# Kernel tuning notes

Measured on AMD Instinct MI355X. Metric: run time of the kernel, lower is better.

Reference implementation:

```python
import jax, jax.numpy as jnp
import numpy as np

INPUT_SIZE = 1024
HIDDEN_SIZE = 1024
BATCH = 8192


def setup_inputs() -> dict:
    key = jax.random.key(0)
    ks = jax.random.split(key, 14)
    stdv = 1.0 / HIDDEN_SIZE ** 0.5
    u = lambda k, shape: jax.random.uniform(k, shape, jnp.float32, -stdv, stdv)
    H, I = HIDDEN_SIZE, INPUT_SIZE
    return {
        "x": jax.random.normal(ks[0], (BATCH, I), jnp.float32),
        "hidden": jax.random.normal(ks[1], (BATCH, H), jnp.float32),
        "weight_xr": u(ks[2], (H, I)),
        "weight_hr": u(ks[3], (H, H)),
        "bias_r": u(ks[4], (H,)),
        "weight_xz": u(ks[5], (H, I)),
        "weight_hz": u(ks[6], (H, H)),
        "bias_z": u(ks[7], (H,)),
        "weight_xh": u(ks[8], (H, I)),
        "weight_hh": u(ks[9], (H, H)),
        "bias_h": u(ks[10], (H,)),
        "weight_c": u(ks[11], (H, I + H)),
        "bias_c": u(ks[12], (H,)),
        "weight_hat_h": u(ks[13], (H, I + H)),
        "bias_hat_h": u(jax.random.fold_in(key, 99), (H,)),
    }


def reference(x, hidden, weight_xr, weight_hr, bias_r, weight_xz, weight_hz, bias_z,
              weight_xh, weight_hh, bias_h, weight_c, bias_c, weight_hat_h, bias_hat_h):
    # combined: [B, I+H]
    combined = jnp.concatenate([x, hidden], axis=1)
    c_t = combined @ weight_c.T + bias_c                      # [B, H]
    a_t = jax.nn.softmax(c_t, axis=1)
    hat_h_t = a_t * jax.nn.relu(combined @ weight_hat_h.T + bias_hat_h)
    r_t = jax.nn.sigmoid(x @ weight_xr.T + bias_r + hidden @ weight_hr.T)
    z_t = jax.nn.sigmoid(x @ weight_xz.T + bias_z + hidden @ weight_hz.T)
    h_tilde = jnp.tanh(x @ weight_xh.T + bias_h + (r_t * hidden) @ weight_hh.T)
    h_t = (1.0 - z_t) * h_tilde + z_t * hidden + hat_h_t
    return h_t
```

## Files before the change

kernel.cpp:

```cpp
#include <hip/hip_runtime.h>

typedef unsigned short ushort_t;
typedef __attribute__((ext_vector_type(8))) short short8;
typedef __attribute__((ext_vector_type(4))) float float4v;
typedef __attribute__((ext_vector_type(4))) ushort_t ushort4v;

#define B_ROWS 8192
#define HDIM   1024
#define GLD    5120

__device__ __forceinline__ float bf2f(ushort_t u) {
    return __uint_as_float(((unsigned)u) << 16);
}
__device__ __forceinline__ ushort_t f2bf(float f) {
    unsigned u = __float_as_uint(f);
    u += 0x7FFFu + ((u >> 16) & 1u);
    return (ushort_t)(u >> 16);
}

__global__ __launch_bounds__(256) void pack_all(
    const float* __restrict__ x, const float* __restrict__ h,
    const float* __restrict__ wc, const float* __restrict__ what,
    const float* __restrict__ wxr, const float* __restrict__ whr,
    const float* __restrict__ wxz, const float* __restrict__ whz,
    const float* __restrict__ wxh, const float* __restrict__ whh,
    ushort_t* __restrict__ A, ushort_t* __restrict__ W,
    ushort_t* __restrict__ Whh)
{
    const int bid = blockIdx.x;
    float4v v;
    ushort_t* dst;
    size_t i4;
    if (bid < 16384) {
        i4 = ((size_t)bid * 256 + threadIdx.x) * 4;
        int c = (int)(i4 & 2047);
        size_t b = i4 >> 11;
        const float* src = (c < 1024) ? (x + b * 1024 + c)
                                      : (h + b * 1024 + (c - 1024));
        v = *(const float4v*)src;
        dst = A + i4;
    } else if (bid < 26624) {
        i4 = ((size_t)(bid - 16384) * 256 + threadIdx.x) * 4;
        int j = (int)(i4 >> 11);
        int k = (int)(i4 & 2047);
        int r = j >> 10, jr = j & 1023;
        if (r == 0) {
            v = *(const float4v*)(wc + (size_t)j * 2048 + k);
        } else if (r == 1) {
            v = *(const float4v*)(what + (size_t)jr * 2048 + k);
        } else if (r == 4) {
            v = (k < 1024) ? *(const float4v*)(wxh + (size_t)jr * 1024 + k)
                           : (float4v){0.f, 0.f, 0.f, 0.f};
        } else {
            const float* p0 = (r == 2) ? wxr : wxz;
            const float* p1 = (r == 2) ? whr : whz;
            const float* p = (k < 1024) ? (p0 + (size_t)jr * 1024 + k)
                                        : (p1 + (size_t)jr * 1024 + (k - 1024));
            v = *(const float4v*)p;
        }
        dst = W + i4;
    } else {
        i4 = ((size_t)(bid - 26624) * 256 + threadIdx.x) * 4;
        v = *(const float4v*)(whh + i4);
        dst = Whh + i4;
    }
    ushort4v o;
#pragma unroll
    for (int t = 0; t < 4; ++t) o[t] = f2bf(v[t]);
    *(ushort4v*)dst = o;
}

__global__ __launch_bounds__(256, 2) void gemm1(
    const ushort_t* __restrict__ A, const ushort_t* __restrict__ B,
    ushort_t* __restrict__ C)
{
    const int bn0 = blockIdx.x * 128;
    const int bm0 = blockIdx.y * 256;
    const int K = (bn0 >= 4096) ? 1024 : 2048;

    __shared__ ushort_t As[256 * 64];
    __shared__ ushort_t Bs[128 * 64];

    const int t = threadIdx.x;
    const int wave = t >> 6, lane = t & 63;
    const int q = lane >> 4, r16 = lane & 15;
    const int lrow8 = lane >> 3;
    const int kswz = ((lane & 7) ^ lrow8) * 8;
    const int xm = (r16 & 7);

    float4v acc[4][8];
#pragma unroll
    for (int i = 0; i < 4; ++i)
#pragma unroll
        for (int j = 0; j < 8; ++j)
            acc[i][j] = {0.f, 0.f, 0.f, 0.f};

    for (int k0 = 0; k0 < K; k0 += 64) {
#pragma unroll
        for (int j = 0; j < 8; ++j) {
            int l = wave * 8 + j;
            const ushort_t* gp = A + (size_t)(bm0 + l * 8 + lrow8) * 2048 + k0 + kswz;
            __builtin_amdgcn_global_load_lds(
                (const __attribute__((address_space(1))) void*)gp,
                (__attribute__((address_space(3))) void*)(As + l * 512),
                16, 0, 0);
        }
#pragma unroll
        for (int j = 0; j < 4; ++j) {
            int l = wave * 4 + j;
            const ushort_t* gp = B + (size_t)(bn0 + l * 8 + lrow8) * 2048 + k0 + kswz;
            __builtin_amdgcn_global_load_lds(
                (const __attribute__((address_space(1))) void*)gp,
                (__attribute__((address_space(3))) void*)(Bs + l * 512),
                16, 0, 0);
        }
        __syncthreads();

#pragma unroll
        for (int kh = 0; kh < 2; ++kh) {
            short8 af[4];
#pragma unroll
            for (int mi = 0; mi < 4; ++mi)
                af[mi] = *(const short8*)
                    &As[(wave * 64 + mi * 16 + r16) * 64 + (((kh * 4 + q) ^ xm) * 8)];
#pragma unroll
            for (int ni = 0; ni < 8; ++ni) {
                short8 bf = *(const short8*)
                    &Bs[(ni * 16 + r16) * 64 + (((kh * 4 + q) ^ xm) * 8)];
#pragma unroll
                for (int mi = 0; mi < 4; ++mi)
                    acc[mi][ni] = __builtin_amdgcn_mfma_f32_16x16x32_bf16(
                        af[mi], bf, acc[mi][ni], 0, 0, 0);
            }
        }
        __syncthreads();
    }

#pragma unroll
    for (int mi = 0; mi < 4; ++mi)
#pragma unroll
        for (int ni = 0; ni < 8; ++ni)
#pragma unroll
            for (int reg = 0; reg < 4; ++reg) {
                int row = bm0 + wave * 64 + mi * 16 + q * 4 + reg;
                int col = bn0 + ni * 16 + r16;
                C[(size_t)row * GLD + col] = f2bf(acc[mi][ni][reg]);
            }
}

__global__ __launch_bounds__(256) void row_pass(
    ushort_t* __restrict__ G, const float* __restrict__ bias_c,
    const float* __restrict__ bias_hat, const float* __restrict__ bias_r,
    const float* __restrict__ hidden, ushort_t* __restrict__ rh)
{
    const int wave = threadIdx.x >> 6, lane = threadIdx.x & 63;
    const size_t row = (size_t)blockIdx.x * 4 + wave;
    ushort_t* g = G + row * GLD;
    const int c0 = lane * 16;

    float cv[16];
    {
        short8 a = *(const short8*)(g + c0);
        short8 b = *(const short8*)(g + c0 + 8);
#pragma unroll
        for (int i = 0; i < 8; ++i) {
            cv[i]     = bf2f((ushort_t)a[i]) + bias_c[c0 + i];
            cv[8 + i] = bf2f((ushort_t)b[i]) + bias_c[c0 + 8 + i];
        }
    }
    float mx = cv[0];
#pragma unroll
    for (int i = 1; i < 16; ++i) mx = fmaxf(mx, cv[i]);
#pragma unroll
    for (int m = 1; m < 64; m <<= 1) mx = fmaxf(mx, __shfl_xor(mx, m));
    float sum = 0.f;
#pragma unroll
    for (int i = 0; i < 16; ++i) { cv[i] = __expf(cv[i] - mx); sum += cv[i]; }
#pragma unroll
    for (int m = 1; m < 64; m <<= 1) sum += __shfl_xor(sum, m);
    const float inv = 1.0f / sum;

    {
        short8 a = *(const short8*)(g + 1024 + c0);
        short8 b = *(const short8*)(g + 1024 + c0 + 8);
        short8 oa, ob;
#pragma unroll
        for (int i = 0; i < 8; ++i) {
            float ha = bf2f((ushort_t)a[i]) + bias_hat[c0 + i];
            float hb = bf2f((ushort_t)b[i]) + bias_hat[c0 + 8 + i];
            oa[i] = (short)f2bf(cv[i] * inv * fmaxf(ha, 0.f));
            ob[i] = (short)f2bf(cv[8 + i] * inv * fmaxf(hb, 0.f));
        }
        *(short8*)(g + c0) = oa;
        *(short8*)(g + c0 + 8) = ob;
    }

    {
        short8 a = *(const short8*)(g + 2048 + c0);
        short8 b = *(const short8*)(g + 2048 + c0 + 8);
        const float* hp = hidden + row * 1024 + c0;
        short8 oa, ob;
#pragma unroll
        for (int i = 0; i < 8; ++i) {
            float ra = 1.0f / (1.0f + __expf(-(bf2f((ushort_t)a[i]) + bias_r[c0 + i])));
            float rb = 1.0f / (1.0f + __expf(-(bf2f((ushort_t)b[i]) + bias_r[c0 + 8 + i])));
            oa[i] = (short)f2bf(ra * hp[i]);
            ob[i] = (short)f2bf(rb * hp[8 + i]);
        }
        ushort_t* rp = rh + row * 1024 + c0;
        *(short8*)rp = oa;
        *(short8*)(rp + 8) = ob;
    }
}

#define CSTRIDE 132
__global__ __launch_bounds__(256) void gemm2_final(
    const ushort_t* __restrict__ A, const ushort_t* __restrict__ B,
    const ushort_t* __restrict__ G, const float* __restrict__ bias_z,
    const float* __restrict__ bias_h, const float* __restrict__ hidden,
    float* __restrict__ out)
{
    const int bn0 = blockIdx.x * 128;
    const int bm0 = blockIdx.y * 64;

    __shared__ ushort_t smem[64 * CSTRIDE];
    ushort_t* As = smem;
    ushort_t* Bs = smem + 2048;

    const int t = threadIdx.x;
    const int wave = t >> 6, lane = t & 63;
    const int wr = wave >> 1, wcq = wave & 1;
    const int q = lane >> 4, r16 = lane & 15;
    const int lrow = lane >> 2;
    const int lcol = (lane & 3) * 8;

    float4v acc[2][4];
#pragma unroll
    for (int i = 0; i < 2; ++i)
#pragma unroll
        for (int j = 0; j < 4; ++j)
            acc[i][j] = {0.f, 0.f, 0.f, 0.f};

    for (int k0 = 0; k0 < 1024; k0 += 32) {
#pragma unroll
        for (int j = 0; j < 3; ++j) {
            int l = wave * 3 + j;
            if (l < 4) {
                const ushort_t* gp = A + (size_t)(bm0 + l * 16 + lrow) * 1024 + k0 + lcol;
                __builtin_amdgcn_global_load_lds(
                    (const __attribute__((address_space(1))) void*)gp,
                    (__attribute__((address_space(3))) void*)(As + l * 512),
                    16, 0, 0);
            } else {
                const ushort_t* gp = B + (size_t)(bn0 + (l - 4) * 16 + lrow) * 1024 + k0 + lcol;
                __builtin_amdgcn_global_load_lds(
                    (const __attribute__((address_space(1))) void*)gp,
                    (__attribute__((address_space(3))) void*)(Bs + (l - 4) * 512),
                    16, 0, 0);
            }
        }
        __syncthreads();

        short8 af[2], bf[4];
#pragma unroll
        for (int mi = 0; mi < 2; ++mi)
            af[mi] = *(const short8*)&As[(wr * 32 + mi * 16 + r16) * 32 + q * 8];
#pragma unroll
        for (int ni = 0; ni < 4; ++ni)
            bf[ni] = *(const short8*)&Bs[(wcq * 64 + ni * 16 + r16) * 32 + q * 8];
#pragma unroll
        for (int mi = 0; mi < 2; ++mi)
#pragma unroll
            for (int ni = 0; ni < 4; ++ni)
                acc[mi][ni] = __builtin_amdgcn_mfma_f32_16x16x32_bf16(
                    af[mi], bf[ni], acc[mi][ni], 0, 0, 0);
        __syncthreads();
    }

#pragma unroll
    for (int mi = 0; mi < 2; ++mi)
#pragma unroll
        for (int ni = 0; ni < 4; ++ni)
#pragma unroll
            for (int reg = 0; reg < 4; ++reg) {
                int rl = wr * 32 + mi * 16 + q * 4 + reg;
                int cl = wcq * 64 + ni * 16 + r16;
                smem[rl * CSTRIDE + cl] = f2bf(acc[mi][ni][reg]);
            }
    __syncthreads();

    const int colL = t & 127;
    const int gc = bn0 + colL;
    const float bz = bias_z[gc];
    const float bh = bias_h[gc];
    const int rbase = t >> 7;
#pragma unroll 4
    for (int pass = 0; pass < 32; ++pass) {
        const int rowL = pass * 2 + rbase;
        const size_t gr = (size_t)(bm0 + rowL);
        const ushort_t* grow = G + gr * GLD;
        float z = 1.0f / (1.0f + __expf(-(bf2f(grow[3072 + gc]) + bz)));
        float targ = bf2f(grow[4096 + gc]) + bh + bf2f(smem[rowL * CSTRIDE + colL]);
        float th = 1.0f - 2.0f / (__expf(2.0f * targ) + 1.0f);
        out[gr * 1024 + gc] =
            (1.0f - z) * th + z * hidden[gr * 1024 + gc] + bf2f(grow[gc]);
    }
}


extern "C" void kernel_launch(void* const* d_in, const int* in_sizes, int n_in,
                              void* d_out, int out_size, void* d_ws, size_t ws_size,
                              hipStream_t stream)
{
    const float* x        = (const float*)d_in[0];
    const float* hidden   = (const float*)d_in[1];
    const float* wxr      = (const float*)d_in[2];
    const float* whr      = (const float*)d_in[3];
    const float* bias_r   = (const float*)d_in[4];
    const float* wxz      = (const float*)d_in[5];
    const float* whz      = (const float*)d_in[6];
    const float* bias_z   = (const float*)d_in[7];
    const float* wxh      = (const float*)d_in[8];
    const float* whh      = (const float*)d_in[9];
    const float* bias_h   = (const float*)d_in[10];
    const float* wc       = (const float*)d_in[11];
    const float* bias_c   = (const float*)d_in[12];
    const float* what     = (const float*)d_in[13];
    const float* bias_hat = (const float*)d_in[14];
    float* out = (float*)d_out;

    char* ws = (char*)d_ws;
    ushort_t* G     = (ushort_t*)(ws);
    ushort_t* Abf   = (ushort_t*)(ws + 83886080);
    ushort_t* Wbf   = (ushort_t*)(ws + 117440512);
    ushort_t* Whhbf = (ushort_t*)(ws + 138412032);
    ushort_t* rhbf  = (ushort_t*)(ws + 140509184);

    pack_all<<<27648, 256, 0, stream>>>(x, hidden, wc, what, wxr, whr, wxz, whz,
                                        wxh, whh, Abf, Wbf, Whhbf);

    gemm1<<<dim3(40, 32), 256, 0, stream>>>(Abf, Wbf, G);

    row_pass<<<B_ROWS / 4, 256, 0, stream>>>(G, bias_c, bias_hat, bias_r, hidden, rhbf);

    gemm2_final<<<dim3(8, 128), 256, 0, stream>>>(rhbf, Whhbf, G, bias_z, bias_h,
                                                  hidden, out);
}
```

Measured before the change: 376.3 us.

## Fuse r-gate epilogue into gemm1, stage stores via LDS, enlarge gemm2 tiles

gemm1 now stages its accumulator tile through shared memory so each thread writes 128-byte contiguous rows instead of scattered 2-byte stores. For the r-gate column block it computes sigmoid(r)*hidden directly and writes rh, so it no longer stores that slice of G and row_pass no longer reads it back. gemm2_final moves to 128x128 tiles with K-step 64 and XOR-swizzled LDS loads, which raises reuse per block but halves the grid and adds register pressure.

```diff
diff --git a/kernel.cpp b/kernel.cpp
--- a/kernel.cpp
+++ b/kernel.cpp
@@ -70,16 +70,19 @@
     *(ushort4v*)dst = o;
 }
 
+#define CS1 136
 __global__ __launch_bounds__(256, 2) void gemm1(
     const ushort_t* __restrict__ A, const ushort_t* __restrict__ B,
-    ushort_t* __restrict__ C)
+    ushort_t* __restrict__ C, const float* __restrict__ hidden,
+    const float* __restrict__ bias_r, ushort_t* __restrict__ rh)
 {
     const int bn0 = blockIdx.x * 128;
     const int bm0 = blockIdx.y * 256;
     const int K = (bn0 >= 4096) ? 1024 : 2048;
 
-    __shared__ ushort_t As[256 * 64];
-    __shared__ ushort_t Bs[128 * 64];
+    __shared__ ushort_t smem[24576];
+    ushort_t* As = smem;
+    ushort_t* Bs = smem + 16384;
 
     const int t = threadIdx.x;
     const int wave = t >> 6, lane = t & 63;
@@ -125,33 +128,64 @@
                     &As[(wave * 64 + mi * 16 + r16) * 64 + (((kh * 4 + q) ^ xm) * 8)];
 #pragma unroll
             for (int ni = 0; ni < 8; ++ni) {
-                short8 bf = *(const short8*)
+                short8 bfv = *(const short8*)
                     &Bs[(ni * 16 + r16) * 64 + (((kh * 4 + q) ^ xm) * 8)];
 #pragma unroll
                 for (int mi = 0; mi < 4; ++mi)
                     acc[mi][ni] = __builtin_amdgcn_mfma_f32_16x16x32_bf16(
-                        af[mi], bf, acc[mi][ni], 0, 0, 0);
-            }
-        }
-        __syncthreads();
-    }
-
-#pragma unroll
-    for (int mi = 0; mi < 4; ++mi)
-#pragma unroll
-        for (int ni = 0; ni < 8; ++ni)
-#pragma unroll
-            for (int reg = 0; reg < 4; ++reg) {
-                int row = bm0 + wave * 64 + mi * 16 + q * 4 + reg;
-                int col = bn0 + ni * 16 + r16;
-                C[(size_t)row * GLD + col] = f2bf(acc[mi][ni][reg]);
-            }
+                        af[mi], bfv, acc[mi][ni], 0, 0, 0);
+            }
+        }
+        __syncthreads();
+    }
+
+    const bool isR = (bn0 >= 2048) && (bn0 < 3072);
+    const int lr = t >> 1;
+    const int co = (t & 1) * 64;
+#pragma unroll
+    for (int half = 0; half < 2; ++half) {
+        if ((wave >> 1) == half) {
+            const int rb = (wave & 1) * 64;
+#pragma unroll
+            for (int mi = 0; mi < 4; ++mi)
+#pragma unroll
+                for (int ni = 0; ni < 8; ++ni)
+#pragma unroll
+                    for (int reg = 0; reg < 4; ++reg)
+                        smem[(rb + mi * 16 + q * 4 + reg) * CS1 + ni * 16 + r16] =
+                            f2bf(acc[mi][ni][reg]);
+        }
+        __syncthreads();
+        const int growi = bm0 + half * 128 + lr;
+        if (!isR) {
+            ushort_t* gdst = C + (size_t)growi * GLD + bn0 + co;
+#pragma unroll
+            for (int j = 0; j < 8; ++j)
+                *(short8*)(gdst + j * 8) = *(const short8*)&smem[lr * CS1 + co + j * 8];
+        } else {
+            const int cb = bn0 - 2048 + co;
+            const float* hp = hidden + (size_t)growi * 1024 + cb;
+            ushort_t* rdst = rh + (size_t)growi * 1024 + cb;
+#pragma unroll
+            for (int j = 0; j < 8; ++j) {
+                short8 v = *(const short8*)&smem[lr * CS1 + co + j * 8];
+                short8 o;
+#pragma unroll
+                for (int i = 0; i < 8; ++i) {
+                    float g = bf2f((ushort_t)v[i]) + bias_r[cb + j * 8 + i];
+                    float s = 1.0f / (1.0f + __expf(-g));
+                    o[i] = (short)f2bf(s * hp[j * 8 + i]);
+                }
+                *(short8*)(rdst + j * 8) = o;
+            }
+        }
+        __syncthreads();
+    }
 }
 
 __global__ __launch_bounds__(256) void row_pass(
     ushort_t* __restrict__ G, const float* __restrict__ bias_c,
-    const float* __restrict__ bias_hat, const float* __restrict__ bias_r,
-    const float* __restrict__ hidden, ushort_t* __restrict__ rh)
+    const float* __restrict__ bias_hat)
 {
     const int wave = threadIdx.x >> 6, lane = threadIdx.x & 63;
     const size_t row = (size_t)blockIdx.x * 4 + wave;
@@ -180,40 +214,21 @@
     for (int m = 1; m < 64; m <<= 1) sum += __shfl_xor(sum, m);
     const float inv = 1.0f / sum;
 
-    {
-        short8 a = *(const short8*)(g + 1024 + c0);
-        short8 b = *(const short8*)(g + 1024 + c0 + 8);
-        short8 oa, ob;
-#pragma unroll
-        for (int i = 0; i < 8; ++i) {
-            float ha = bf2f((ushort_t)a[i]) + bias_hat[c0 + i];
-            float hb = bf2f((ushort_t)b[i]) + bias_hat[c0 + 8 + i];
-            oa[i] = (short)f2bf(cv[i] * inv * fmaxf(ha, 0.f));
-            ob[i] = (short)f2bf(cv[8 + i] * inv * fmaxf(hb, 0.f));
-        }
-        *(short8*)(g + c0) = oa;
-        *(short8*)(g + c0 + 8) = ob;
-    }
-
-    {
-        short8 a = *(const short8*)(g + 2048 + c0);
-        short8 b = *(const short8*)(g + 2048 + c0 + 8);
-        const float* hp = hidden + row * 1024 + c0;
-        short8 oa, ob;
-#pragma unroll
-        for (int i = 0; i < 8; ++i) {
-            float ra = 1.0f / (1.0f + __expf(-(bf2f((ushort_t)a[i]) + bias_r[c0 + i])));
-            float rb = 1.0f / (1.0f + __expf(-(bf2f((ushort_t)b[i]) + bias_r[c0 + 8 + i])));
-            oa[i] = (short)f2bf(ra * hp[i]);
-            ob[i] = (short)f2bf(rb * hp[8 + i]);
-        }
-        ushort_t* rp = rh + row * 1024 + c0;
-        *(short8*)rp = oa;
-        *(short8*)(rp + 8) = ob;
-    }
-}
-
-#define CSTRIDE 132
+    short8 a = *(const short8*)(g + 1024 + c0);
+    short8 b = *(const short8*)(g + 1024 + c0 + 8);
+    short8 oa, ob;
+#pragma unroll
+    for (int i = 0; i < 8; ++i) {
+        float ha = bf2f((ushort_t)a[i]) + bias_hat[c0 + i];
+        float hb = bf2f((ushort_t)b[i]) + bias_hat[c0 + 8 + i];
+        oa[i] = (short)f2bf(cv[i] * inv * fmaxf(ha, 0.f));
+        ob[i] = (short)f2bf(cv[8 + i] * inv * fmaxf(hb, 0.f));
+    }
+    *(short8*)(g + c0) = oa;
+    *(short8*)(g + c0 + 8) = ob;
+}
+
+#define CS2 132
 __global__ __launch_bounds__(256) void gemm2_final(
     const ushort_t* __restrict__ A, const ushort_t* __restrict__ B,
     const ushort_t* __restrict__ G, const float* __restrict__ bias_z,
@@ -221,71 +236,76 @@
     float* __restrict__ out)
 {
     const int bn0 = blockIdx.x * 128;
-    const int bm0 = blockIdx.y * 64;
-
-    __shared__ ushort_t smem[64 * CSTRIDE];
+    const int bm0 = blockIdx.y * 128;
+
+    __shared__ ushort_t smem[128 * CS2];
     ushort_t* As = smem;
-    ushort_t* Bs = smem + 2048;
+    ushort_t* Bs = smem + 8192;
 
     const int t = threadIdx.x;
     const int wave = t >> 6, lane = t & 63;
     const int wr = wave >> 1, wcq = wave & 1;
     const int q = lane >> 4, r16 = lane & 15;
-    const int lrow = lane >> 2;
-    const int lcol = (lane & 3) * 8;
-
-    float4v acc[2][4];
-#pragma unroll
-    for (int i = 0; i < 2; ++i)
+    const int lrow8 = lane >> 3;
+    const int kswz = ((lane & 7) ^ lrow8) * 8;
+    const int xm = (r16 & 7);
+
+    float4v acc[4][4];
+#pragma unroll
+    for (int i = 0; i < 4; ++i)
 #pragma unroll
         for (int j = 0; j < 4; ++j)
             acc[i][j] = {0.f, 0.f, 0.f, 0.f};
 
-    for (int k0 = 0; k0 < 1024; k0 += 32) {
-#pragma unroll
-        for (int j = 0; j < 3; ++j) {
-            int l = wave * 3 + j;
-            if (l < 4) {
-                const ushort_t* gp = A + (size_t)(bm0 + l * 16 + lrow) * 1024 + k0 + lcol;
+    for (int k0 = 0; k0 < 1024; k0 += 64) {
+#pragma unroll
+        for (int j = 0; j < 8; ++j) {
+            int l = wave * 8 + j;
+            if (l < 16) {
+                const ushort_t* gp = A + (size_t)(bm0 + l * 8 + lrow8) * 1024 + k0 + kswz;
                 __builtin_amdgcn_global_load_lds(
                     (const __attribute__((address_space(1))) void*)gp,
                     (__attribute__((address_space(3))) void*)(As + l * 512),
                     16, 0, 0);
             } else {
-                const ushort_t* gp = B + (size_t)(bn0 + (l - 4) * 16 + lrow) * 1024 + k0 + lcol;
+                const ushort_t* gp = B + (size_t)(bn0 + (l - 16) * 8 + lrow8) * 1024 + k0 + kswz;
                 __builtin_amdgcn_global_load_lds(
                     (const __attribute__((address_space(1))) void*)gp,
-                    (__attribute__((address_space(3))) void*)(Bs + (l - 4) * 512),
+                    (__attribute__((address_space(3))) void*)(Bs + (l - 16) * 512),
                     16, 0, 0);
             }
         }
         __syncthreads();
 
-        short8 af[2], bf[4];
-#pragma unroll
-        for (int mi = 0; mi < 2; ++mi)
-            af[mi] = *(const short8*)&As[(wr * 32 + mi * 16 + r16) * 32 + q * 8];
+#pragma unroll
+        for (int kh = 0; kh < 2; ++kh) {
+            short8 af[4];
+#pragma unroll
+            for (int mi = 0; mi < 4; ++mi)
+                af[mi] = *(const short8*)
+                    &As[(wr * 64 + mi * 16 + r16) * 64 + (((kh * 4 + q) ^ xm) * 8)];
+#pragma unroll
+            for (int ni = 0; ni < 4; ++ni) {
+                short8 bfv = *(const short8*)
+                    &Bs[(wcq * 64 + ni * 16 + r16) * 64 + (((kh * 4 + q) ^ xm) * 8)];
+#pragma unroll
+                for (int mi = 0; mi < 4; ++mi)
+                    acc[mi][ni] = __builtin_amdgcn_mfma_f32_16x16x32_bf16(
+                        af[mi], bfv, acc[mi][ni], 0, 0, 0);
+            }
+        }
+        __syncthreads();
+    }
+
+#pragma unroll
+    for (int mi = 0; mi < 4; ++mi)
 #pragma unroll
         for (int ni = 0; ni < 4; ++ni)
-            bf[ni] = *(const short8*)&Bs[(wcq * 64 + ni * 16 + r16) * 32 + q * 8];
-#pragma unroll
-        for (int mi = 0; mi < 2; ++mi)
-#pragma unroll
-            for (int ni = 0; ni < 4; ++ni)
-                acc[mi][ni] = __builtin_amdgcn_mfma_f32_16x16x32_bf16(
-                    af[mi], bf[ni], acc[mi][ni], 0, 0, 0);
-        __syncthreads();
-    }
-
-#pragma unroll
-    for (int mi = 0; mi < 2; ++mi)
-#pragma unroll
-        for (int ni = 0; ni < 4; ++ni)
 #pragma unroll
             for (int reg = 0; reg < 4; ++reg) {
-                int rl = wr * 32 + mi * 16 + q * 4 + reg;
+                int rl = wr * 64 + mi * 16 + q * 4 + reg;
                 int cl = wcq * 64 + ni * 16 + r16;
-                smem[rl * CSTRIDE + cl] = f2bf(acc[mi][ni][reg]);
+                smem[rl * CS2 + cl] = f2bf(acc[mi][ni][reg]);
             }
     __syncthreads();
 
@@ -295,12 +315,12 @@
     const float bh = bias_h[gc];
     const int rbase = t >> 7;
 #pragma unroll 4
-    for (int pass = 0; pass < 32; ++pass) {
+    for (int pass = 0; pass < 64; ++pass) {
         const int rowL = pass * 2 + rbase;
         const size_t gr = (size_t)(bm0 + rowL);
         const ushort_t* grow = G + gr * GLD;
         float z = 1.0f / (1.0f + __expf(-(bf2f(grow[3072 + gc]) + bz)));
-        float targ = bf2f(grow[4096 + gc]) + bh + bf2f(smem[rowL * CSTRIDE + colL]);
+        float targ = bf2f(grow[4096 + gc]) + bh + bf2f(smem[rowL * CS2 + colL]);
         float th = 1.0f - 2.0f / (__expf(2.0f * targ) + 1.0f);
         out[gr * 1024 + gc] =
             (1.0f - z) * th + z * hidden[gr * 1024 + gc] + bf2f(grow[gc]);
@@ -339,10 +359,10 @@
     pack_all<<<27648, 256, 0, stream>>>(x, hidden, wc, what, wxr, whr, wxz, whz,
                                         wxh, whh, Abf, Wbf, Whhbf);
 
-    gemm1<<<dim3(40, 32), 256, 0, stream>>>(Abf, Wbf, G);
-
-    row_pass<<<B_ROWS / 4, 256, 0, stream>>>(G, bias_c, bias_hat, bias_r, hidden, rhbf);
-
-    gemm2_final<<<dim3(8, 128), 256, 0, stream>>>(rhbf, Whhbf, G, bias_z, bias_h,
-                                                  hidden, out);
-}
+    gemm1<<<dim3(40, 32), 256, 0, stream>>>(Abf, Wbf, G, hidden, bias_r, rhbf);
+
+    row_pass<<<B_ROWS / 4, 256, 0, stream>>>(G, bias_c, bias_hat);
+
+    gemm2_final<<<dim3(8, 64), 256, 0, stream>>>(rhbf, Whhbf, G, bias_z, bias_h,
+                                                 hidden, out);
+}
```

After: 388.5 us. 1.03x slower.
